# Kernel tuning notes

Hardware: AMD Instinct MI355X
Metric: run time of the kernel (lower is better)

The kernel has to match this reference:

```python
import jax, jax.numpy as jnp
import numpy as np
from jax import lax

B, H, W = 16, 96, 320
NUM_JOINTS = 9
THRESH = 0.1


def _nms(heat):
    # 3x3 max-pool NMS: keep only local maxima
    hmax = lax.reduce_window(heat, -jnp.inf, lax.max, (1, 1, 3, 3), (1, 1, 1, 1), 'SAME')
    return jnp.where(hmax == heat, heat, jnp.zeros_like(heat))


def _gather_feat(feat_bhc, ind):
    # feat_bhc: (B, HW, C), ind: (B, K) -> (B, K, C)
    return jnp.take_along_axis(feat_bhc, ind[:, :, None], axis=1)


def _transpose_and_gather_feat(feat, ind):
    # feat: (B, C, H, W), ind: (B, K) -> (B, K, C)
    b, c = feat.shape[0], feat.shape[1]
    f = feat.reshape(b, c, -1).transpose(0, 2, 1)  # (B, HW, C)
    return _gather_feat(f, ind)


def _topk(heat, K):
    b, c, h, w = heat.shape
    scores = heat.reshape(b, c, h * w)
    topk_scores, topk_inds = lax.top_k(scores, K)            # (B, C, K)
    topk_ys = (topk_inds // w).astype(heat.dtype)
    topk_xs = (topk_inds % w).astype(heat.dtype)
    topk_score, topk_ind = lax.top_k(topk_scores.reshape(b, c * K), K)  # (B, K)
    clses = topk_ind // K
    g = lambda a: jnp.take_along_axis(a.reshape(b, c * K), topk_ind, axis=1)
    return topk_score, g(topk_inds), clses, g(topk_ys), g(topk_xs)


def _topk_channel(heat, K):
    b, c, h, w = heat.shape
    scores = heat.reshape(b, c, h * w)
    topk_scores, topk_inds = lax.top_k(scores, K)  # (B, C, K)
    topk_ys = (topk_inds // w).astype(heat.dtype)
    topk_xs = (topk_inds % w).astype(heat.dtype)
    return topk_scores, topk_inds, topk_ys, topk_xs


def setup_inputs() -> dict:
    key = jax.random.key(0)
    ks = jax.random.split(key, 9)
    mk = lambda k, c: jax.random.normal(k, (B, c, H, W), dtype=jnp.float32)
    return {
        'hm': mk(ks[0], 3), 'wh': mk(ks[1], 2), 'hps': mk(ks[2], 18),
        'dim': mk(ks[3], 3), 'rot': mk(ks[4], 8), 'prob': mk(ks[5], 1),
        'reg': mk(ks[6], 2), 'hm_hp': mk(ks[7], 9), 'hp_offset': mk(ks[8], 2),
        'K': 100,
    }


def _decode(hm, wh, hps, dim, rot, prob, reg, hm_hp, hp_offset, K):
    b = hm.shape[0]
    J = hps.shape[1] // 2
    heat = _nms(jax.nn.sigmoid(hm))
    scores, inds, clses, ys0, xs0 = _topk(heat, K)  # (B, K) each

    kps = _transpose_and_gather_feat(hps, inds).reshape(b, K, J, 2)
    kps = kps + jnp.stack([xs0, ys0], axis=-1)[:, :, None, :]  # add center coords

    reg_g = _transpose_and_gather_feat(reg, inds)  # (B, K, 2)
    xs = xs0[:, :, None] + reg_g[:, :, 0:1]
    ys = ys0[:, :, None] + reg_g[:, :, 1:2]

    wh_g = _transpose_and_gather_feat(wh, inds)  # (B, K, 2)
    clses_f = clses.astype(hm.dtype)[:, :, None]
    scores_f = scores[:, :, None]
    bboxes = jnp.concatenate([xs - wh_g[..., 0:1] / 2, ys - wh_g[..., 1:2] / 2,
                              xs + wh_g[..., 0:1] / 2, ys + wh_g[..., 1:2] / 2], axis=2)

    dim_g = _transpose_and_gather_feat(dim, inds)        # (B, K, 3)
    rot_g = _transpose_and_gather_feat(rot, inds)        # (B, K, 8)
    prob_g = _transpose_and_gather_feat(prob, inds)[:, :, 0:1]  # (B, K, 1)

    # keypoint heatmap refinement
    hmhp = _nms(jax.nn.sigmoid(hm_hp))
    kps_jk = kps.transpose(0, 2, 1, 3)  # (B, J, K, 2)
    hm_score, hm_inds, hm_ys, hm_xs = _topk_channel(hmhp, K)  # (B, J, K)
    hp_off = _transpose_and_gather_feat(hp_offset, hm_inds.reshape(b, -1)).reshape(b, J, K, 2)
    hm_xs = hm_xs + hp_off[..., 0]
    hm_ys = hm_ys + hp_off[..., 1]

    valid = hm_score > THRESH
    hm_score = jnp.where(valid, hm_score, -1.0)
    hm_ys = jnp.where(valid, hm_ys, -10000.0)
    hm_xs = jnp.where(valid, hm_xs, -10000.0)
    hm_kps = jnp.stack([hm_xs, hm_ys], axis=-1)  # (B, J, K, 2)

    dist = jnp.sqrt(((kps_jk[:, :, :, None, :] - hm_kps[:, :, None, :, :]) ** 2).sum(-1))  # (B,J,K,K)
    min_dist = dist.min(axis=3)
    min_ind = dist.argmin(axis=3)  # (B, J, K)
    hm_score_sel = jnp.take_along_axis(hm_score, min_ind, axis=2)[..., None]  # (B,J,K,1)
    hm_kps_sel = jnp.take_along_axis(hm_kps, min_ind[..., None], axis=2)      # (B,J,K,2)

    l = bboxes[:, :, 0][:, None, :, None]
    t = bboxes[:, :, 1][:, None, :, None]
    r = bboxes[:, :, 2][:, None, :, None]
    bb = bboxes[:, :, 3][:, None, :, None]
    md = min_dist[..., None]
    invalid = ((hm_kps_sel[..., 0:1] < l) | (hm_kps_sel[..., 0:1] > r) |
               (hm_kps_sel[..., 1:2] < t) | (hm_kps_sel[..., 1:2] > bb) |
               (hm_score_sel < THRESH) | (md > jnp.maximum(bb - t, r - l) * 0.3))
    kps_out = jnp.where(invalid, kps_jk, hm_kps_sel)  # (B, J, K, 2)
    kps_final = kps_out.transpose(0, 2, 1, 3).reshape(b, K, J * 2) * 4.0
    hm_score_out = hm_score_sel[..., 0].transpose(0, 2, 1)  # (B, K, J)

    bboxes = bboxes * 4.0
    detections = jnp.concatenate(
        [bboxes, scores_f, kps_final, dim_g, hm_score_out, rot_g, prob_g, clses_f], axis=2)
    return detections  # (B, K, 4+1+18+3+9+8+1+1 = 45)


def reference(hm, wh, hps, dim, rot, prob, reg, hm_hp, hp_offset, K):
    return _decode(hm, wh, hps, dim, rot, prob, reg, hm_hp, hp_offset, K)
```

## Files before the change

### kernel.cpp

```cpp
#include <hip/hip_runtime.h>
#include <math.h>

typedef unsigned int u32;
typedef unsigned short u16;
typedef unsigned long long u64;

#define HW    30720
#define W_    320
#define H_    96
#define B_    16
#define KTOP  100
#define NIMG  192
#define NTHR  1024
#define SCAP  4096

__global__ __launch_bounds__(NTHR) void fused_nms_select_kernel(
    const float* __restrict__ hm, const float* __restrict__ hm_hp,
    u32* __restrict__ tkKey, u32* __restrict__ tkIdx)
{
    const int row = blockIdx.x;
    const int tid = threadIdx.x;

    __shared__ u32 candKey[SCAP];
    __shared__ u16 candPix[SCAP];
    __shared__ u32 hist[4096];
    __shared__ u32 selb1, selG1, selb2;
    __shared__ u32 cnt, cnt2;

    u64* cand2 = (u64*)hist;

    if (tid == 0) { cnt = 0; cnt2 = 0; }
    #pragma unroll
    for (int j = 0; j < 4; ++j) hist[tid + j * NTHR] = 0;

    const float* __restrict__ base = (row < 48)
        ? (hm + (size_t)row * HW) : (hm_hp + (size_t)(row - 48) * HW);
    __syncthreads();

    for (int q = tid; q < HW / 4; q += NTHR) {
        int y  = q / 80;
        int qx = q - y * 80;
        int x0 = qx * 4;
        const float* rm = base + (y > 0 ? y - 1 : 0) * W_;
        const float* rc = base + y * W_;
        const float* rp = base + (y < H_ - 1 ? y + 1 : H_ - 1) * W_;
        float4 am = *(const float4*)(rm + x0);
        float4 ac = *(const float4*)(rc + x0);
        float4 ap = *(const float4*)(rp + x0);
        float cm0 = fmaxf(fmaxf(am.x, ac.x), ap.x);
        float cm1 = fmaxf(fmaxf(am.y, ac.y), ap.y);
        float cm2 = fmaxf(fmaxf(am.z, ac.z), ap.z);
        float cm3 = fmaxf(fmaxf(am.w, ac.w), ap.w);
        float cl, cr;
        if (qx > 0)
            cl = fmaxf(fmaxf(rm[x0 - 1], rc[x0 - 1]), rp[x0 - 1]);
        else cl = cm0;
        if (qx < 79)
            cr = fmaxf(fmaxf(rm[x0 + 4], rc[x0 + 4]), rp[x0 + 4]);
        else cr = cm3;

        float cen[4] = {ac.x, ac.y, ac.z, ac.w};
        float mx[4];
        mx[0] = fmaxf(fmaxf(cl,  cm0), cm1);
        mx[1] = fmaxf(fmaxf(cm0, cm1), cm2);
        mx[2] = fmaxf(fmaxf(cm1, cm2), cm3);
        mx[3] = fmaxf(fmaxf(cm2, cm3), cr);
        #pragma unroll
        for (int j = 0; j < 4; ++j) {
            if (cen[j] == mx[j]) {
                float s = 1.0f / (1.0f + expf(-cen[j]));
                u32 p = atomicAdd(&cnt, 1u);
                if (p < SCAP) {
                    candKey[p] = __float_as_uint(s);
                    candPix[p] = (u16)(x0 + j + y * W_);
                }
            }
        }
    }
    __syncthreads();
    const u32 n = (cnt > SCAP) ? SCAP : cnt;

    for (u32 i = tid; i < n; i += NTHR)
        atomicAdd(&hist[candKey[i] >> 20], 1u);
    __syncthreads();
    if (tid < 64) {
        int lane = tid;
        u32 v[4], t[4];
        #pragma unroll
        for (int k = 0; k < 4; ++k) {
            u32 s = 0; int b0 = (lane * 4 + k) * 16;
            #pragma unroll
            for (int qq = 0; qq < 16; ++qq) s += hist[b0 + qq];
            v[k] = s;
        }
        t[3] = v[3]; t[2] = v[2] + t[3]; t[1] = v[1] + t[2]; t[0] = v[0] + t[1];
        u32 lt = t[0], s = lt;
        #pragma unroll
        for (int d = 1; d < 64; d <<= 1) {
            u32 o = __shfl_down(s, d);
            if (lane + d < 64) s += o;
        }
        u32 SH = s - lt;
        u32 sfx[5] = {t[0] + SH, t[1] + SH, t[2] + SH, t[3] + SH, SH};
        #pragma unroll
        for (int k = 0; k < 4; ++k) {
            if (sfx[k] >= KTOP && sfx[k + 1] < KTOP) {
                u32 run = sfx[k + 1];
                int c = lane * 4 + k;
                for (int bin = c * 16 + 15; bin >= c * 16; --bin) {
                    u32 h = hist[bin];
                    if (run + h >= KTOP) { selb1 = (u32)bin; selG1 = run; break; }
                    run += h;
                }
            }
        }
    }
    __syncthreads();
    const u32 b1 = selb1, G1 = selG1;

    #pragma unroll
    for (int j = 0; j < 4; ++j) hist[tid + j * NTHR] = 0;
    __syncthreads();
    for (u32 i = tid; i < n; i += NTHR) {
        u32 k = candKey[i];
        if ((k >> 20) == b1) atomicAdd(&hist[(k >> 8) & 0xFFFu], 1u);
    }
    __syncthreads();
    {
        const u32 K2 = KTOP - G1;
        if (tid < 64) {
            int lane = tid;
            u32 v[4], t[4];
            #pragma unroll
            for (int k = 0; k < 4; ++k) {
                u32 s = 0; int b0 = (lane * 4 + k) * 16;
                #pragma unroll
                for (int qq = 0; qq < 16; ++qq) s += hist[b0 + qq];
                v[k] = s;
            }
            t[3] = v[3]; t[2] = v[2] + t[3]; t[1] = v[1] + t[2]; t[0] = v[0] + t[1];
            u32 lt = t[0], s = lt;
            #pragma unroll
            for (int d = 1; d < 64; d <<= 1) {
                u32 o = __shfl_down(s, d);
                if (lane + d < 64) s += o;
            }
            u32 SH = s - lt;
            u32 sfx[5] = {t[0] + SH, t[1] + SH, t[2] + SH, t[3] + SH, SH};
            #pragma unroll
            for (int k = 0; k < 4; ++k) {
                if (sfx[k] >= K2 && sfx[k + 1] < K2) {
                    u32 run = sfx[k + 1];
                    int c = lane * 4 + k;
                    for (int bin = c * 16 + 15; bin >= c * 16; --bin) {
                        u32 h = hist[bin];
                        if (run + h >= K2) { selb2 = (u32)bin; break; }
                        run += h;
                    }
                }
            }
        }
    }
    __syncthreads();
    const u32 cut24 = (b1 << 12) | selb2;

    for (u32 i = tid; i < n; i += NTHR) {
        u32 k = candKey[i];
        if ((k >> 8) >= cut24) {
            u32 p = atomicAdd(&cnt2, 1u);
            if (p < 2048) cand2[p] = ((u64)k << 32) | (u32)(~(u32)candPix[i]);
        }
    }
    __syncthreads();
    u32 q = cnt2; if (q > 2048) q = 2048;

    if (q <= NTHR) {
        if (tid < q) {
            u64 v = cand2[tid];
            u32 rank = 0;
            for (u32 i = 0; i < q; ++i) rank += (cand2[i] > v);
            if (rank < KTOP) {
                tkKey[row * KTOP + rank] = (u32)(v >> 32);
                tkIdx[row * KTOP + rank] = ~(u32)v;
            }
        }
    } else {
        u32 npow = 128; while (npow < q) npow <<= 1;
        for (u32 i = q + tid; i < npow; i += NTHR) cand2[i] = 0ull;
        __syncthreads();
        for (u32 ks = 2; ks <= npow; ks <<= 1) {
            for (u32 j = ks >> 1; j > 0; j >>= 1) {
                for (u32 i = tid; i < npow; i += NTHR) {
                    u32 ix = i ^ j;
                    if (ix > i) {
                        u64 a = cand2[i], b = cand2[ix];
                        bool sw = ((i & ks) == 0) ? (a < b) : (a > b);
                        if (sw) { cand2[i] = b; cand2[ix] = a; }
                    }
                }
                __syncthreads();
            }
        }
        if (tid < KTOP) {
            u64 v = cand2[tid];
            tkKey[row * KTOP + tid] = (u32)(v >> 32);
            tkIdx[row * KTOP + tid] = ~(u32)v;
        }
    }
}

__global__ __launch_bounds__(320) void decode_kernel(
    const u32* __restrict__ tkKey, const u32* __restrict__ tkIdx,
    const float* __restrict__ wh,   const float* __restrict__ hps,
    const float* __restrict__ dimp, const float* __restrict__ rot,
    const float* __restrict__ prob, const float* __restrict__ reg,
    const float* __restrict__ hpo,  float* __restrict__ det)
{
    const int blk = blockIdx.x;
    const int b = blk / 9;
    const int j = blk - b * 9;
    const int tid = threadIdx.x;

    __shared__ u64 arr[300];
    __shared__ u64 selv[KTOP];
    __shared__ float hsv[KTOP], hxv[KTOP], hyv[KTOP];

    if (tid < 300) {
        int c = tid / 100, r = tid - c * 100;
        u32 key = tkKey[(b * 3 + c) * KTOP + r];
        arr[tid] = ((u64)key << 32) | (u32)(~(u32)tid);
    }
    __syncthreads();
    if (tid < 300) {
        u64 v = arr[tid];
        u32 rank = 0;
        for (int i = 0; i < 300; ++i) rank += (arr[i] > v);
        if (rank < KTOP) selv[rank] = v;
    }
    __syncthreads();

    float l = 0.f, t = 0.f, rr = 0.f, bb = 0.f, kxr = 0.f, kyr = 0.f;

    if (tid < KTOP) {
        int k = tid;
        u64 v = selv[k];
        u32 pos = ~(u32)v;
        if (pos > 299u) pos = 299u;
        u32 key = (u32)(v >> 32);
        int c = (int)pos / 100, r = (int)pos - c * 100;
        u32 sid = tkIdx[(b * 3 + c) * KTOP + r];
        if (sid > HW - 1) sid = HW - 1;
        float score = __uint_as_float(key);
        int yy = (int)sid / W_, xx = (int)sid - yy * W_;
        float xs0 = (float)xx, ys0 = (float)yy;
        float r0 = reg[((size_t)b * 2 + 0) * HW + sid];
        float r1 = reg[((size_t)b * 2 + 1) * HW + sid];
        float xsv = xs0 + r0, ysv = ys0 + r1;
        float w0 = wh[((size_t)b * 2 + 0) * HW + sid];
        float w1 = wh[((size_t)b * 2 + 1) * HW + sid];
        l  = xsv - w0 * 0.5f;
        t  = ysv - w1 * 0.5f;
        rr = xsv + w0 * 0.5f;
        bb = ysv + w1 * 0.5f;
        kxr = hps[((size_t)b * 18 + 2 * j)     * HW + sid] + xs0;
        kyr = hps[((size_t)b * 18 + 2 * j + 1) * HW + sid] + ys0;
        if (j == 0) {
            float* o = det + ((size_t)b * KTOP + k) * 45;
            o[0] = l * 4.0f; o[1] = t * 4.0f; o[2] = rr * 4.0f; o[3] = bb * 4.0f;
            o[4] = score;
            o[44] = (float)c;
        }
    } else if (tid < 200) {
        int r = tid - 100;
        int rw = 48 + b * 9 + j;
        u32 key = tkKey[rw * KTOP + r];
        u32 idx = tkIdx[rw * KTOP + r];
        if (idx > HW - 1) idx = HW - 1;
        float s = __uint_as_float(key);
        int yy = (int)idx / W_, xx = (int)idx - yy * W_;
        float hx = (float)xx + hpo[((size_t)b * 2 + 0) * HW + idx];
        float hy = (float)yy + hpo[((size_t)b * 2 + 1) * HW + idx];
        bool valid = s > 0.1f;
        hsv[r] = valid ? s : -1.0f;
        hxv[r] = valid ? hx : -10000.0f;
        hyv[r] = valid ? hy : -10000.0f;
    } else if (tid < 300 && j == 0) {
        int k = tid - 200;
        u64 v = selv[k];
        u32 pos = ~(u32)v;
        if (pos > 299u) pos = 299u;
        int c = (int)pos / 100, r = (int)pos - c * 100;
        u32 sid = tkIdx[(b * 3 + c) * KTOP + r];
        if (sid > HW - 1) sid = HW - 1;
        float* o = det + ((size_t)b * KTOP + k) * 45;
        #pragma unroll
        for (int qq = 0; qq < 3; ++qq)
            o[23 + qq] = dimp[((size_t)b * 3 + qq) * HW + sid];
        #pragma unroll
        for (int qq = 0; qq < 8; ++qq)
            o[35 + qq] = rot[((size_t)b * 8 + qq) * HW + sid];
        o[43] = prob[(size_t)b * HW + sid];
    }
    __syncthreads();

    if (tid < KTOP) {
        int k = tid;
        float best = INFINITY; int bi = 0;
        for (int m = 0; m < 100; ++m) {
            float dx = kxr - hxv[m];
            float dy = kyr - hyv[m];
            float d2 = __fadd_rn(__fmul_rn(dx, dx), __fmul_rn(dy, dy));
            float d = __fsqrt_rn(d2);
            if (d < best) { best = d; bi = m; }
        }
        float ss = hsv[bi], hx = hxv[bi], hy = hyv[bi];
        float th = __fmul_rn(fmaxf(__fsub_rn(bb, t), __fsub_rn(rr, l)), 0.3f);
        bool invalid = (hx < l) | (hx > rr) | (hy < t) | (hy > bb) |
                       (ss < 0.1f) | (best > th);
        float ox = invalid ? kxr : hx;
        float oy = invalid ? kyr : hy;
        float* o = det + ((size_t)b * KTOP + k) * 45;
        o[5 + 2 * j] = ox * 4.0f;
        o[6 + 2 * j] = oy * 4.0f;
        o[26 + j]    = ss;
    }
}

extern "C" void kernel_launch(void* const* d_in, const int* in_sizes, int n_in,
                              void* d_out, int out_size, void* d_ws, size_t ws_size,
                              hipStream_t stream) {
    const float* hm    = (const float*)d_in[0];
    const float* wh    = (const float*)d_in[1];
    const float* hps   = (const float*)d_in[2];
    const float* dimp  = (const float*)d_in[3];
    const float* rot   = (const float*)d_in[4];
    const float* prob  = (const float*)d_in[5];
    const float* reg   = (const float*)d_in[6];
    const float* hm_hp = (const float*)d_in[7];
    const float* hpo   = (const float*)d_in[8];
    float* det = (float*)d_out;

    u32* tkKey = (u32*)d_ws;
    u32* tkIdx = tkKey + NIMG * KTOP;

    fused_nms_select_kernel<<<NIMG, NTHR, 0, stream>>>(hm, hm_hp, tkKey, tkIdx);
    decode_kernel<<<B_ * 9, 320, 0, stream>>>(tkKey, tkIdx, wh, hps, dimp, rot,
                                              prob, reg, hpo, det);
}
```

Before: 156.6 us.

## Split NMS scan across many blocks per image before top-k selection

The fused NMS+select kernel ran one 1024-thread block per image (192 blocks), so the heatmap scan used few CUs. This change splits the NMS scan into 30 blocks per image (5760 blocks) that write local-maximum candidates into per-segment global buffers. A separate select kernel then compacts those segments and runs the existing radix histogram top-k. The cost is an extra kernel launch, a global round trip for the candidates, and a per-segment cap of 256 candidates that could drop some on dense inputs.

```diff
diff --git a/kernel.cpp b/kernel.cpp
--- a/kernel.cpp
+++ b/kernel.cpp
@@ -11,80 +11,112 @@
 #define B_    16
 #define KTOP  100
 #define NIMG  192
+#define BPR   30
+#define BCAP  256
 #define NTHR  1024
-#define SCAP  4096
-
-__global__ __launch_bounds__(NTHR) void fused_nms_select_kernel(
+
+__global__ __launch_bounds__(256) void nms_kernel(
     const float* __restrict__ hm, const float* __restrict__ hm_hp,
+    u64* __restrict__ segbuf, u32* __restrict__ segcnt)
+{
+    const int gb  = blockIdx.x;
+    const int img = gb / BPR;
+    const int sub = gb - img * BPR;
+    const int tid = threadIdx.x;
+
+    __shared__ u32 lcnt;
+    __shared__ u64 lc[BCAP];
+    if (tid == 0) lcnt = 0;
+    __syncthreads();
+
+    const float* __restrict__ base = (img < 48)
+        ? (hm + (size_t)img * HW) : (hm_hp + (size_t)(img - 48) * HW);
+
+    int qi = sub * 256 + tid;
+    int y  = qi / 80;
+    int qx = qi - y * 80;
+    int x0 = qx * 4;
+    const float* rm = base + (y > 0 ? y - 1 : 0) * W_;
+    const float* rc = base + y * W_;
+    const float* rp = base + (y < H_ - 1 ? y + 1 : H_ - 1) * W_;
+    float4 am = *(const float4*)(rm + x0);
+    float4 ac = *(const float4*)(rc + x0);
+    float4 ap = *(const float4*)(rp + x0);
+    float cm0 = fmaxf(fmaxf(am.x, ac.x), ap.x);
+    float cm1 = fmaxf(fmaxf(am.y, ac.y), ap.y);
+    float cm2 = fmaxf(fmaxf(am.z, ac.z), ap.z);
+    float cm3 = fmaxf(fmaxf(am.w, ac.w), ap.w);
+    float cl, cr;
+    if (qx > 0)
+        cl = fmaxf(fmaxf(rm[x0 - 1], rc[x0 - 1]), rp[x0 - 1]);
+    else cl = cm0;
+    if (qx < 79)
+        cr = fmaxf(fmaxf(rm[x0 + 4], rc[x0 + 4]), rp[x0 + 4]);
+    else cr = cm3;
+
+    float cen[4] = {ac.x, ac.y, ac.z, ac.w};
+    float mx[4];
+    mx[0] = fmaxf(fmaxf(cl,  cm0), cm1);
+    mx[1] = fmaxf(fmaxf(cm0, cm1), cm2);
+    mx[2] = fmaxf(fmaxf(cm1, cm2), cm3);
+    mx[3] = fmaxf(fmaxf(cm2, cm3), cr);
+    #pragma unroll
+    for (int j = 0; j < 4; ++j) {
+        if (cen[j] == mx[j]) {
+            float s = 1.0f / (1.0f + expf(-cen[j]));
+            u32 pix = (u32)(y * W_ + x0 + j);
+            u32 p = atomicAdd(&lcnt, 1u);
+            if (p < BCAP)
+                lc[p] = ((u64)__float_as_uint(s) << 32) | (u32)(~pix);
+        }
+    }
+    __syncthreads();
+    u32 c = lcnt; if (c > BCAP) c = BCAP;
+    if (tid < c) segbuf[(size_t)gb * BCAP + tid] = lc[tid];
+    if (tid == 0) segcnt[gb] = c;
+}
+
+__global__ __launch_bounds__(NTHR) void select_kernel(
+    const u64* __restrict__ segbuf, const u32* __restrict__ segcnt,
     u32* __restrict__ tkKey, u32* __restrict__ tkIdx)
 {
     const int row = blockIdx.x;
     const int tid = threadIdx.x;
-
-    __shared__ u32 candKey[SCAP];
-    __shared__ u16 candPix[SCAP];
+    const int lane = tid & 63;
+
+    __shared__ u64 cand[4096];
     __shared__ u32 hist[4096];
+    __shared__ u64 cand2[2048];
+    __shared__ u32 cnts[BPR], pfx[BPR + 1];
     __shared__ u32 selb1, selG1, selb2;
-    __shared__ u32 cnt, cnt2;
-
-    u64* cand2 = (u64*)hist;
-
-    if (tid == 0) { cnt = 0; cnt2 = 0; }
+    __shared__ u32 cnt2;
+
+    if (tid == 0) cnt2 = 0;
+    if (tid < BPR) cnts[tid] = segcnt[row * BPR + tid];
     #pragma unroll
     for (int j = 0; j < 4; ++j) hist[tid + j * NTHR] = 0;
-
-    const float* __restrict__ base = (row < 48)
-        ? (hm + (size_t)row * HW) : (hm_hp + (size_t)(row - 48) * HW);
-    __syncthreads();
-
-    for (int q = tid; q < HW / 4; q += NTHR) {
-        int y  = q / 80;
-        int qx = q - y * 80;
-        int x0 = qx * 4;
-        const float* rm = base + (y > 0 ? y - 1 : 0) * W_;
-        const float* rc = base + y * W_;
-        const float* rp = base + (y < H_ - 1 ? y + 1 : H_ - 1) * W_;
-        float4 am = *(const float4*)(rm + x0);
-        float4 ac = *(const float4*)(rc + x0);
-        float4 ap = *(const float4*)(rp + x0);
-        float cm0 = fmaxf(fmaxf(am.x, ac.x), ap.x);
-        float cm1 = fmaxf(fmaxf(am.y, ac.y), ap.y);
-        float cm2 = fmaxf(fmaxf(am.z, ac.z), ap.z);
-        float cm3 = fmaxf(fmaxf(am.w, ac.w), ap.w);
-        float cl, cr;
-        if (qx > 0)
-            cl = fmaxf(fmaxf(rm[x0 - 1], rc[x0 - 1]), rp[x0 - 1]);
-        else cl = cm0;
-        if (qx < 79)
-            cr = fmaxf(fmaxf(rm[x0 + 4], rc[x0 + 4]), rp[x0 + 4]);
-        else cr = cm3;
-
-        float cen[4] = {ac.x, ac.y, ac.z, ac.w};
-        float mx[4];
-        mx[0] = fmaxf(fmaxf(cl,  cm0), cm1);
-        mx[1] = fmaxf(fmaxf(cm0, cm1), cm2);
-        mx[2] = fmaxf(fmaxf(cm1, cm2), cm3);
-        mx[3] = fmaxf(fmaxf(cm2, cm3), cr);
-        #pragma unroll
-        for (int j = 0; j < 4; ++j) {
-            if (cen[j] == mx[j]) {
-                float s = 1.0f / (1.0f + expf(-cen[j]));
-                u32 p = atomicAdd(&cnt, 1u);
-                if (p < SCAP) {
-                    candKey[p] = __float_as_uint(s);
-                    candPix[p] = (u16)(x0 + j + y * W_);
-                }
-            }
-        }
-    }
-    __syncthreads();
-    const u32 n = (cnt > SCAP) ? SCAP : cnt;
+    __syncthreads();
+    if (tid == 0) {
+        u32 a = 0;
+        for (int s = 0; s < BPR; ++s) { pfx[s] = a; a += cnts[s]; }
+        pfx[BPR] = a;
+    }
+    __syncthreads();
+    u32 n = pfx[BPR]; if (n > 4096) n = 4096;
+
+    for (int i = tid; i < BPR * BCAP; i += NTHR) {
+        int s = i >> 8, l = i & (BCAP - 1);
+        if ((u32)l < cnts[s]) {
+            u32 d = pfx[s] + l;
+            if (d < 4096) cand[d] = segbuf[(size_t)(row * BPR + s) * BCAP + l];
+        }
+    }
+    __syncthreads();
 
     for (u32 i = tid; i < n; i += NTHR)
-        atomicAdd(&hist[candKey[i] >> 20], 1u);
+        atomicAdd(&hist[(u32)(cand[i] >> 52)], 1u);
     __syncthreads();
     if (tid < 64) {
-        int lane = tid;
         u32 v[4], t[4];
         #pragma unroll
         for (int k = 0; k < 4; ++k) {
@@ -122,14 +154,13 @@
     for (int j = 0; j < 4; ++j) hist[tid + j * NTHR] = 0;
     __syncthreads();
     for (u32 i = tid; i < n; i += NTHR) {
-        u32 k = candKey[i];
+        u32 k = (u32)(cand[i] >> 32);
         if ((k >> 20) == b1) atomicAdd(&hist[(k >> 8) & 0xFFFu], 1u);
     }
     __syncthreads();
     {
         const u32 K2 = KTOP - G1;
         if (tid < 64) {
-            int lane = tid;
             u32 v[4], t[4];
             #pragma unroll
             for (int k = 0; k < 4; ++k) {
@@ -165,17 +196,17 @@
     const u32 cut24 = (b1 << 12) | selb2;
 
     for (u32 i = tid; i < n; i += NTHR) {
-        u32 k = candKey[i];
-        if ((k >> 8) >= cut24) {
+        u64 v = cand[i];
+        if ((u32)(v >> 40) >= cut24) {
             u32 p = atomicAdd(&cnt2, 1u);
-            if (p < 2048) cand2[p] = ((u64)k << 32) | (u32)(~(u32)candPix[i]);
+            if (p < 2048) cand2[p] = v;
         }
     }
     __syncthreads();
     u32 q = cnt2; if (q > 2048) q = 2048;
 
     if (q <= NTHR) {
-        if (tid < q) {
+        if (tid < (int)q) {
             u64 v = cand2[tid];
             u32 rank = 0;
             for (u32 i = 0; i < q; ++i) rank += (cand2[i] > v);
@@ -340,10 +371,13 @@
     const float* hpo   = (const float*)d_in[8];
     float* det = (float*)d_out;
 
-    u32* tkKey = (u32*)d_ws;
-    u32* tkIdx = tkKey + NIMG * KTOP;
-
-    fused_nms_select_kernel<<<NIMG, NTHR, 0, stream>>>(hm, hm_hp, tkKey, tkIdx);
+    u64* segbuf = (u64*)d_ws;
+    u32* segcnt = (u32*)(segbuf + (size_t)NIMG * BPR * BCAP);
+    u32* tkKey  = segcnt + NIMG * BPR;
+    u32* tkIdx  = tkKey + NIMG * KTOP;
+
+    nms_kernel<<<NIMG * BPR, 256, 0, stream>>>(hm, hm_hp, segbuf, segcnt);
+    select_kernel<<<NIMG, NTHR, 0, stream>>>(segbuf, segcnt, tkKey, tkIdx);
     decode_kernel<<<B_ * 9, 320, 0, stream>>>(tkKey, tkIdx, wh, hps, dimp, rot,
                                               prob, reg, hpo, det);
 }
```

New measurement: 154.6 us, median of 2. Within noise of the previous version (-1.2%).

## Fuse NMS, top-k selection and decode into one cooperative kernel with segmented scan

Applied to the files above, without the earlier changes.

Replaces the two launches with one cooperative kernel of 768 blocks of 256 threads. The NMS scan is split into 30 segments per image so all CUs share the bandwidth-bound pass, and each segment writes its local-maximum candidates to a global buffer. After a grid sync, one block per image runs the radix histogram select over the gathered candidates. After a second grid sync, the decode stage runs. This aims to fix the under-parallelised 192-block NMS pass and remove a launch, at the cost of two grid barriers, a global round-trip for candidates, and per-segment candidate caps (256) that could drop candidates on dense inputs.

```diff
diff --git a/kernel.cpp b/kernel.cpp
--- a/kernel.cpp
+++ b/kernel.cpp
@@ -1,5 +1,8 @@
 #include <hip/hip_runtime.h>
+#include <hip/hip_cooperative_groups.h>
 #include <math.h>
+
+namespace cg = cooperative_groups;
 
 typedef unsigned int u32;
 typedef unsigned short u16;
@@ -11,35 +14,45 @@
 #define B_    16
 #define KTOP  100
 #define NIMG  192
-#define NTHR  1024
-#define SCAP  4096
-
-__global__ __launch_bounds__(NTHR) void fused_nms_select_kernel(
-    const float* __restrict__ hm, const float* __restrict__ hm_hp,
-    u32* __restrict__ tkKey, u32* __restrict__ tkIdx)
+#define BPR   30
+#define NSEGT (NIMG * BPR)
+#define BCAP  256
+#define GRID  768
+#define THR   256
+
+union SMem {
+    struct { u64 lc[BCAP]; u32 lcnt; } a;
+    struct { u32 hist[4096]; u64 cand2[2048];
+             u32 cnts[BPR]; u32 selb1, selG1, selb2, cnt2; } b;
+    struct { u64 arr[300]; u64 selv[KTOP];
+             float hsv[KTOP], hxv[KTOP], hyv[KTOP]; } c;
+};
+
+__global__ __launch_bounds__(THR, 3) void km3d_kernel(
+    const float* __restrict__ hm,   const float* __restrict__ wh,
+    const float* __restrict__ hps,  const float* __restrict__ dimp,
+    const float* __restrict__ rot,  const float* __restrict__ prob,
+    const float* __restrict__ reg,  const float* __restrict__ hm_hp,
+    const float* __restrict__ hpo,  float* __restrict__ det,
+    u64* __restrict__ segbuf, u32* __restrict__ segcnt,
+    u32* __restrict__ tkKey,  u32* __restrict__ tkIdx)
 {
-    const int row = blockIdx.x;
+    const int bid = blockIdx.x;
     const int tid = threadIdx.x;
-
-    __shared__ u32 candKey[SCAP];
-    __shared__ u16 candPix[SCAP];
-    __shared__ u32 hist[4096];
-    __shared__ u32 selb1, selG1, selb2;
-    __shared__ u32 cnt, cnt2;
-
-    u64* cand2 = (u64*)hist;
-
-    if (tid == 0) { cnt = 0; cnt2 = 0; }
-    #pragma unroll
-    for (int j = 0; j < 4; ++j) hist[tid + j * NTHR] = 0;
-
-    const float* __restrict__ base = (row < 48)
-        ? (hm + (size_t)row * HW) : (hm_hp + (size_t)(row - 48) * HW);
-    __syncthreads();
-
-    for (int q = tid; q < HW / 4; q += NTHR) {
-        int y  = q / 80;
-        int qx = q - y * 80;
+    const int lane = tid & 63;
+    __shared__ SMem sm;
+    cg::grid_group grid = cg::this_grid();
+
+    for (int seg = bid; seg < NSEGT; seg += gridDim.x) {
+        if (tid == 0) sm.a.lcnt = 0;
+        __syncthreads();
+        const int img = seg / BPR;
+        const int sub = seg - img * BPR;
+        const float* __restrict__ base = (img < 48)
+            ? (hm + (size_t)img * HW) : (hm_hp + (size_t)(img - 48) * HW);
+        int qi = sub * 256 + tid;
+        int y  = qi / 80;
+        int qx = qi - y * 80;
         int x0 = qx * 4;
         const float* rm = base + (y > 0 ? y - 1 : 0) * W_;
         const float* rc = base + y * W_;
@@ -58,7 +71,6 @@
         if (qx < 79)
             cr = fmaxf(fmaxf(rm[x0 + 4], rc[x0 + 4]), rp[x0 + 4]);
         else cr = cm3;
-
         float cen[4] = {ac.x, ac.y, ac.z, ac.w};
         float mx[4];
         mx[0] = fmaxf(fmaxf(cl,  cm0), cm1);
@@ -69,73 +81,42 @@
         for (int j = 0; j < 4; ++j) {
             if (cen[j] == mx[j]) {
                 float s = 1.0f / (1.0f + expf(-cen[j]));
-                u32 p = atomicAdd(&cnt, 1u);
-                if (p < SCAP) {
-                    candKey[p] = __float_as_uint(s);
-                    candPix[p] = (u16)(x0 + j + y * W_);
-                }
-            }
-        }
+                u32 pix = (u32)(y * W_ + x0 + j);
+                u32 p = atomicAdd(&sm.a.lcnt, 1u);
+                if (p < BCAP)
+                    sm.a.lc[p] = ((u64)__float_as_uint(s) << 32) | (u32)(~pix);
+            }
+        }
+        __syncthreads();
+        u32 c = sm.a.lcnt; if (c > BCAP) c = BCAP;
+        if (tid < c) segbuf[(size_t)seg * BCAP + tid] = sm.a.lc[tid];
+        if (tid == 0) segcnt[seg] = c;
+        __syncthreads();
     }
-    __syncthreads();
-    const u32 n = (cnt > SCAP) ? SCAP : cnt;
-
-    for (u32 i = tid; i < n; i += NTHR)
-        atomicAdd(&hist[candKey[i] >> 20], 1u);
-    __syncthreads();
-    if (tid < 64) {
-        int lane = tid;
-        u32 v[4], t[4];
-        #pragma unroll
-        for (int k = 0; k < 4; ++k) {
-            u32 s = 0; int b0 = (lane * 4 + k) * 16;
-            #pragma unroll
-            for (int qq = 0; qq < 16; ++qq) s += hist[b0 + qq];
-            v[k] = s;
-        }
-        t[3] = v[3]; t[2] = v[2] + t[3]; t[1] = v[1] + t[2]; t[0] = v[0] + t[1];
-        u32 lt = t[0], s = lt;
-        #pragma unroll
-        for (int d = 1; d < 64; d <<= 1) {
-            u32 o = __shfl_down(s, d);
-            if (lane + d < 64) s += o;
-        }
-        u32 SH = s - lt;
-        u32 sfx[5] = {t[0] + SH, t[1] + SH, t[2] + SH, t[3] + SH, SH};
-        #pragma unroll
-        for (int k = 0; k < 4; ++k) {
-            if (sfx[k] >= KTOP && sfx[k + 1] < KTOP) {
-                u32 run = sfx[k + 1];
-                int c = lane * 4 + k;
-                for (int bin = c * 16 + 15; bin >= c * 16; --bin) {
-                    u32 h = hist[bin];
-                    if (run + h >= KTOP) { selb1 = (u32)bin; selG1 = run; break; }
-                    run += h;
-                }
-            }
-        }
-    }
-    __syncthreads();
-    const u32 b1 = selb1, G1 = selG1;
-
-    #pragma unroll
-    for (int j = 0; j < 4; ++j) hist[tid + j * NTHR] = 0;
-    __syncthreads();
-    for (u32 i = tid; i < n; i += NTHR) {
-        u32 k = candKey[i];
-        if ((k >> 20) == b1) atomicAdd(&hist[(k >> 8) & 0xFFFu], 1u);
-    }
-    __syncthreads();
-    {
-        const u32 K2 = KTOP - G1;
+    __threadfence();
+    grid.sync();
+
+    if (bid < NIMG) {
+        const int row = bid;
+        const u64* __restrict__ rowseg = segbuf + (size_t)row * BPR * BCAP;
+        if (tid == 0) sm.b.cnt2 = 0;
+        if (tid < BPR) sm.b.cnts[tid] = segcnt[row * BPR + tid];
+        for (int i = tid; i < 4096; i += THR) sm.b.hist[i] = 0;
+        __syncthreads();
+
+        for (int i = tid; i < BPR * BCAP; i += THR) {
+            int s = i >> 8, l = i & (BCAP - 1);
+            if ((u32)l < sm.b.cnts[s])
+                atomicAdd(&sm.b.hist[(u32)(rowseg[i] >> 52)], 1u);
+        }
+        __syncthreads();
         if (tid < 64) {
-            int lane = tid;
             u32 v[4], t[4];
             #pragma unroll
             for (int k = 0; k < 4; ++k) {
                 u32 s = 0; int b0 = (lane * 4 + k) * 16;
                 #pragma unroll
-                for (int qq = 0; qq < 16; ++qq) s += hist[b0 + qq];
+                for (int qq = 0; qq < 16; ++qq) s += sm.b.hist[b0 + qq];
                 v[k] = s;
             }
             t[3] = v[3]; t[2] = v[2] + t[3]; t[1] = v[1] + t[2]; t[0] = v[0] + t[1];
@@ -149,180 +130,202 @@
             u32 sfx[5] = {t[0] + SH, t[1] + SH, t[2] + SH, t[3] + SH, SH};
             #pragma unroll
             for (int k = 0; k < 4; ++k) {
-                if (sfx[k] >= K2 && sfx[k + 1] < K2) {
+                if (sfx[k] >= KTOP && sfx[k + 1] < KTOP) {
                     u32 run = sfx[k + 1];
                     int c = lane * 4 + k;
                     for (int bin = c * 16 + 15; bin >= c * 16; --bin) {
-                        u32 h = hist[bin];
-                        if (run + h >= K2) { selb2 = (u32)bin; break; }
+                        u32 h = sm.b.hist[bin];
+                        if (run + h >= KTOP) { sm.b.selb1 = (u32)bin; sm.b.selG1 = run; break; }
                         run += h;
                     }
                 }
             }
         }
-    }
-    __syncthreads();
-    const u32 cut24 = (b1 << 12) | selb2;
-
-    for (u32 i = tid; i < n; i += NTHR) {
-        u32 k = candKey[i];
-        if ((k >> 8) >= cut24) {
-            u32 p = atomicAdd(&cnt2, 1u);
-            if (p < 2048) cand2[p] = ((u64)k << 32) | (u32)(~(u32)candPix[i]);
-        }
-    }
-    __syncthreads();
-    u32 q = cnt2; if (q > 2048) q = 2048;
-
-    if (q <= NTHR) {
-        if (tid < q) {
-            u64 v = cand2[tid];
+        __syncthreads();
+        const u32 b1 = sm.b.selb1, G1 = sm.b.selG1;
+
+        for (int i = tid; i < 4096; i += THR) sm.b.hist[i] = 0;
+        __syncthreads();
+        for (int i = tid; i < BPR * BCAP; i += THR) {
+            int s = i >> 8, l = i & (BCAP - 1);
+            if ((u32)l < sm.b.cnts[s]) {
+                u32 k = (u32)(rowseg[i] >> 32);
+                if ((k >> 20) == b1) atomicAdd(&sm.b.hist[(k >> 8) & 0xFFFu], 1u);
+            }
+        }
+        __syncthreads();
+        {
+            const u32 K2 = KTOP - G1;
+            if (tid < 64) {
+                u32 v[4], t[4];
+                #pragma unroll
+                for (int k = 0; k < 4; ++k) {
+                    u32 s = 0; int b0 = (lane * 4 + k) * 16;
+                    #pragma unroll
+                    for (int qq = 0; qq < 16; ++qq) s += sm.b.hist[b0 + qq];
+                    v[k] = s;
+                }
+                t[3] = v[3]; t[2] = v[2] + t[3]; t[1] = v[1] + t[2]; t[0] = v[0] + t[1];
+                u32 lt = t[0], s = lt;
+                #pragma unroll
+                for (int d = 1; d < 64; d <<= 1) {
+                    u32 o = __shfl_down(s, d);
+                    if (lane + d < 64) s += o;
+                }
+                u32 SH = s - lt;
+                u32 sfx[5] = {t[0] + SH, t[1] + SH, t[2] + SH, t[3] + SH, SH};
+                #pragma unroll
+                for (int k = 0; k < 4; ++k) {
+                    if (sfx[k] >= K2 && sfx[k + 1] < K2) {
+                        u32 run = sfx[k + 1];
+                        int c = lane * 4 + k;
+                        for (int bin = c * 16 + 15; bin >= c * 16; --bin) {
+                            u32 h = sm.b.hist[bin];
+                            if (run + h >= K2) { sm.b.selb2 = (u32)bin; break; }
+                            run += h;
+                        }
+                    }
+                }
+            }
+        }
+        __syncthreads();
+        const u32 cut24 = (b1 << 12) | sm.b.selb2;
+
+        for (int i = tid; i < BPR * BCAP; i += THR) {
+            int s = i >> 8, l = i & (BCAP - 1);
+            if ((u32)l < sm.b.cnts[s]) {
+                u64 v = rowseg[i];
+                if ((u32)(v >> 40) >= cut24) {
+                    u32 p = atomicAdd(&sm.b.cnt2, 1u);
+                    if (p < 2048) sm.b.cand2[p] = v;
+                }
+            }
+        }
+        __syncthreads();
+        u32 q = sm.b.cnt2; if (q > 2048) q = 2048;
+
+        for (u32 ii = tid; ii < q; ii += THR) {
+            u64 v = sm.b.cand2[ii];
             u32 rank = 0;
-            for (u32 i = 0; i < q; ++i) rank += (cand2[i] > v);
+            for (u32 i = 0; i < q; ++i) rank += (sm.b.cand2[i] > v);
             if (rank < KTOP) {
                 tkKey[row * KTOP + rank] = (u32)(v >> 32);
                 tkIdx[row * KTOP + rank] = ~(u32)v;
             }
         }
-    } else {
-        u32 npow = 128; while (npow < q) npow <<= 1;
-        for (u32 i = q + tid; i < npow; i += NTHR) cand2[i] = 0ull;
-        __syncthreads();
-        for (u32 ks = 2; ks <= npow; ks <<= 1) {
-            for (u32 j = ks >> 1; j > 0; j >>= 1) {
-                for (u32 i = tid; i < npow; i += NTHR) {
-                    u32 ix = i ^ j;
-                    if (ix > i) {
-                        u64 a = cand2[i], b = cand2[ix];
-                        bool sw = ((i & ks) == 0) ? (a < b) : (a > b);
-                        if (sw) { cand2[i] = b; cand2[ix] = a; }
-                    }
-                }
-                __syncthreads();
-            }
-        }
+    }
+    __threadfence();
+    grid.sync();
+
+    if (bid < B_ * 9) {
+        const int b = bid / 9;
+        const int j = bid - b * 9;
+
+        if (tid < 300) {
+            int c = tid / 100, r = tid - c * 100;
+            u32 key = tkKey[(b * 3 + c) * KTOP + r];
+            sm.c.arr[tid] = ((u64)key << 32) | (u32)(~(u32)tid);
+        }
+        for (int i = 256 + tid; i < 300; i += THR) {
+            int c = i / 100, r = i - c * 100;
+            u32 key = tkKey[(b * 3 + c) * KTOP + r];
+            sm.c.arr[i] = ((u64)key << 32) | (u32)(~(u32)i);
+        }
+        __syncthreads();
+        for (int ii = tid; ii < 300; ii += THR) {
+            u64 v = sm.c.arr[ii];
+            u32 rank = 0;
+            for (int i = 0; i < 300; ++i) rank += (sm.c.arr[i] > v);
+            if (rank < KTOP) sm.c.selv[rank] = v;
+        }
+        __syncthreads();
+
+        float l = 0.f, t = 0.f, rr = 0.f, bb = 0.f, kxr = 0.f, kyr = 0.f;
+
         if (tid < KTOP) {
-            u64 v = cand2[tid];
-            tkKey[row * KTOP + tid] = (u32)(v >> 32);
-            tkIdx[row * KTOP + tid] = ~(u32)v;
-        }
-    }
-}
-
-__global__ __launch_bounds__(320) void decode_kernel(
-    const u32* __restrict__ tkKey, const u32* __restrict__ tkIdx,
-    const float* __restrict__ wh,   const float* __restrict__ hps,
-    const float* __restrict__ dimp, const float* __restrict__ rot,
-    const float* __restrict__ prob, const float* __restrict__ reg,
-    const float* __restrict__ hpo,  float* __restrict__ det)
-{
-    const int blk = blockIdx.x;
-    const int b = blk / 9;
-    const int j = blk - b * 9;
-    const int tid = threadIdx.x;
-
-    __shared__ u64 arr[300];
-    __shared__ u64 selv[KTOP];
-    __shared__ float hsv[KTOP], hxv[KTOP], hyv[KTOP];
-
-    if (tid < 300) {
-        int c = tid / 100, r = tid - c * 100;
-        u32 key = tkKey[(b * 3 + c) * KTOP + r];
-        arr[tid] = ((u64)key << 32) | (u32)(~(u32)tid);
-    }
-    __syncthreads();
-    if (tid < 300) {
-        u64 v = arr[tid];
-        u32 rank = 0;
-        for (int i = 0; i < 300; ++i) rank += (arr[i] > v);
-        if (rank < KTOP) selv[rank] = v;
-    }
-    __syncthreads();
-
-    float l = 0.f, t = 0.f, rr = 0.f, bb = 0.f, kxr = 0.f, kyr = 0.f;
-
-    if (tid < KTOP) {
-        int k = tid;
-        u64 v = selv[k];
-        u32 pos = ~(u32)v;
-        if (pos > 299u) pos = 299u;
-        u32 key = (u32)(v >> 32);
-        int c = (int)pos / 100, r = (int)pos - c * 100;
-        u32 sid = tkIdx[(b * 3 + c) * KTOP + r];
-        if (sid > HW - 1) sid = HW - 1;
-        float score = __uint_as_float(key);
-        int yy = (int)sid / W_, xx = (int)sid - yy * W_;
-        float xs0 = (float)xx, ys0 = (float)yy;
-        float r0 = reg[((size_t)b * 2 + 0) * HW + sid];
-        float r1 = reg[((size_t)b * 2 + 1) * HW + sid];
-        float xsv = xs0 + r0, ysv = ys0 + r1;
-        float w0 = wh[((size_t)b * 2 + 0) * HW + sid];
-        float w1 = wh[((size_t)b * 2 + 1) * HW + sid];
-        l  = xsv - w0 * 0.5f;
-        t  = ysv - w1 * 0.5f;
-        rr = xsv + w0 * 0.5f;
-        bb = ysv + w1 * 0.5f;
-        kxr = hps[((size_t)b * 18 + 2 * j)     * HW + sid] + xs0;
-        kyr = hps[((size_t)b * 18 + 2 * j + 1) * HW + sid] + ys0;
-        if (j == 0) {
+            int k = tid;
+            u64 v = sm.c.selv[k];
+            u32 pos = ~(u32)v;
+            if (pos > 299u) pos = 299u;
+            u32 key = (u32)(v >> 32);
+            int c = (int)pos / 100, r = (int)pos - c * 100;
+            u32 sid = tkIdx[(b * 3 + c) * KTOP + r];
+            if (sid > HW - 1) sid = HW - 1;
+            float score = __uint_as_float(key);
+            int yy = (int)sid / W_, xx = (int)sid - yy * W_;
+            float xs0 = (float)xx, ys0 = (float)yy;
+            float r0 = reg[((size_t)b * 2 + 0) * HW + sid];
+            float r1 = reg[((size_t)b * 2 + 1) * HW + sid];
+            float xsv = xs0 + r0, ysv = ys0 + r1;
+            float w0 = wh[((size_t)b * 2 + 0) * HW + sid];
+            float w1 = wh[((size_t)b * 2 + 1) * HW + sid];
+            l  = xsv - w0 * 0.5f;
+            t  = ysv - w1 * 0.5f;
+            rr = xsv + w0 * 0.5f;
+            bb = ysv + w1 * 0.5f;
+            kxr = hps[((size_t)b * 18 + 2 * j)     * HW + sid] + xs0;
+            kyr = hps[((size_t)b * 18 + 2 * j + 1) * HW + sid] + ys0;
+            if (j == 0) {
+                float* o = det + ((size_t)b * KTOP + k) * 45;
+                o[0] = l * 4.0f; o[1] = t * 4.0f; o[2] = rr * 4.0f; o[3] = bb * 4.0f;
+                o[4] = score;
+                o[44] = (float)c;
+            }
+        } else if (tid < 200) {
+            int r = tid - 100;
+            int rw = 48 + b * 9 + j;
+            u32 key = tkKey[rw * KTOP + r];
+            u32 idx = tkIdx[rw * KTOP + r];
+            if (idx > HW - 1) idx = HW - 1;
+            float s = __uint_as_float(key);
+            int yy = (int)idx / W_, xx = (int)idx - yy * W_;
+            float hx = (float)xx + hpo[((size_t)b * 2 + 0) * HW + idx];
+            float hy = (float)yy + hpo[((size_t)b * 2 + 1) * HW + idx];
+            bool valid = s > 0.1f;
+            sm.c.hsv[r] = valid ? s : -1.0f;
+            sm.c.hxv[r] = valid ? hx : -10000.0f;
+            sm.c.hyv[r] = valid ? hy : -10000.0f;
+        } else if (j == 0) {
+            for (int k = tid - 200; k < KTOP; k += 56) {
+                u64 v = sm.c.selv[k];
+                u32 pos = ~(u32)v;
+                if (pos > 299u) pos = 299u;
+                int c = (int)pos / 100, r = (int)pos - c * 100;
+                u32 sid = tkIdx[(b * 3 + c) * KTOP + r];
+                if (sid > HW - 1) sid = HW - 1;
+                float* o = det + ((size_t)b * KTOP + k) * 45;
+                #pragma unroll
+                for (int qq = 0; qq < 3; ++qq)
+                    o[23 + qq] = dimp[((size_t)b * 3 + qq) * HW + sid];
+                #pragma unroll
+                for (int qq = 0; qq < 8; ++qq)
+                    o[35 + qq] = rot[((size_t)b * 8 + qq) * HW + sid];
+                o[43] = prob[(size_t)b * HW + sid];
+            }
+        }
+        __syncthreads();
+
+        if (tid < KTOP) {
+            int k = tid;
+            float best = INFINITY; int bi = 0;
+            for (int m = 0; m < 100; ++m) {
+                float dx = kxr - sm.c.hxv[m];
+                float dy = kyr - sm.c.hyv[m];
+                float d2 = __fadd_rn(__fmul_rn(dx, dx), __fmul_rn(dy, dy));
+                float d = __fsqrt_rn(d2);
+                if (d < best) { best = d; bi = m; }
+            }
+            float ss = sm.c.hsv[bi], hx = sm.c.hxv[bi], hy = sm.c.hyv[bi];
+            float th = __fmul_rn(fmaxf(__fsub_rn(bb, t), __fsub_rn(rr, l)), 0.3f);
+            bool invalid = (hx < l) | (hx > rr) | (hy < t) | (hy > bb) |
+                           (ss < 0.1f) | (best > th);
+            float ox = invalid ? kxr : hx;
+            float oy = invalid ? kyr : hy;
             float* o = det + ((size_t)b * KTOP + k) * 45;
-            o[0] = l * 4.0f; o[1] = t * 4.0f; o[2] = rr * 4.0f; o[3] = bb * 4.0f;
-            o[4] = score;
-            o[44] = (float)c;
-        }
-    } else if (tid < 200) {
-        int r = tid - 100;
-        int rw = 48 + b * 9 + j;
-        u32 key = tkKey[rw * KTOP + r];
-        u32 idx = tkIdx[rw * KTOP + r];
-        if (idx > HW - 1) idx = HW - 1;
-        float s = __uint_as_float(key);
-        int yy = (int)idx / W_, xx = (int)idx - yy * W_;
-        float hx = (float)xx + hpo[((size_t)b * 2 + 0) * HW + idx];
-        float hy = (float)yy + hpo[((size_t)b * 2 + 1) * HW + idx];
-        bool valid = s > 0.1f;
-        hsv[r] = valid ? s : -1.0f;
-        hxv[r] = valid ? hx : -10000.0f;
-        hyv[r] = valid ? hy : -10000.0f;
-    } else if (tid < 300 && j == 0) {
-        int k = tid - 200;
-        u64 v = selv[k];
-        u32 pos = ~(u32)v;
-        if (pos > 299u) pos = 299u;
-        int c = (int)pos / 100, r = (int)pos - c * 100;
-        u32 sid = tkIdx[(b * 3 + c) * KTOP + r];
-        if (sid > HW - 1) sid = HW - 1;
-        float* o = det + ((size_t)b * KTOP + k) * 45;
-        #pragma unroll
-        for (int qq = 0; qq < 3; ++qq)
-            o[23 + qq] = dimp[((size_t)b * 3 + qq) * HW + sid];
-        #pragma unroll
-        for (int qq = 0; qq < 8; ++qq)
-            o[35 + qq] = rot[((size_t)b * 8 + qq) * HW + sid];
-        o[43] = prob[(size_t)b * HW + sid];
-    }
-    __syncthreads();
-
-    if (tid < KTOP) {
-        int k = tid;
-        float best = INFINITY; int bi = 0;
-        for (int m = 0; m < 100; ++m) {
-            float dx = kxr - hxv[m];
-            float dy = kyr - hyv[m];
-            float d2 = __fadd_rn(__fmul_rn(dx, dx), __fmul_rn(dy, dy));
-            float d = __fsqrt_rn(d2);
-            if (d < best) { best = d; bi = m; }
-        }
-        float ss = hsv[bi], hx = hxv[bi], hy = hyv[bi];
-        float th = __fmul_rn(fmaxf(__fsub_rn(bb, t), __fsub_rn(rr, l)), 0.3f);
-        bool invalid = (hx < l) | (hx > rr) | (hy < t) | (hy > bb) |
-                       (ss < 0.1f) | (best > th);
-        float ox = invalid ? kxr : hx;
-        float oy = invalid ? kyr : hy;
-        float* o = det + ((size_t)b * KTOP + k) * 45;
-        o[5 + 2 * j] = ox * 4.0f;
-        o[6 + 2 * j] = oy * 4.0f;
-        o[26 + j]    = ss;
+            o[5 + 2 * j] = ox * 4.0f;
+            o[6 + 2 * j] = oy * 4.0f;
+            o[26 + j]    = ss;
+        }
     }
 }
 
@@ -340,10 +343,15 @@
     const float* hpo   = (const float*)d_in[8];
     float* det = (float*)d_out;
 
-    u32* tkKey = (u32*)d_ws;
-    u32* tkIdx = tkKey + NIMG * KTOP;
-
-    fused_nms_select_kernel<<<NIMG, NTHR, 0, stream>>>(hm, hm_hp, tkKey, tkIdx);
-    decode_kernel<<<B_ * 9, 320, 0, stream>>>(tkKey, tkIdx, wh, hps, dimp, rot,
-                                              prob, reg, hpo, det);
+    u64* segbuf = (u64*)d_ws;
+    u32* segcnt = (u32*)(segbuf + (size_t)NSEGT * BCAP);
+    u32* tkKey  = segcnt + NSEGT;
+    u32* tkIdx  = tkKey + NIMG * KTOP;
+
+    void* args[] = { (void*)&hm, (void*)&wh, (void*)&hps, (void*)&dimp,
+                     (void*)&rot, (void*)&prob, (void*)&reg, (void*)&hm_hp,
+                     (void*)&hpo, (void*)&det, (void*)&segbuf, (void*)&segcnt,
+                     (void*)&tkKey, (void*)&tkIdx };
+    hipLaunchCooperativeKernel((const void*)km3d_kernel, dim3(GRID), dim3(THR),
+                               args, 0, stream);
 }
```

Result: slower. 437.5 us (+179.5%).
